# Optimization experiments

Measured on AMD Instinct MI355X. Metric: run time of the kernel, lower is better.

The kernel has to match this reference:

```python
import jax, jax.numpy as jnp
import numpy as np
from jax import lax

B, T, I, H = 256, 256, 512, 512


def setup_inputs() -> dict:
    key = jax.random.key(0)
    ks = jax.random.split(key, 7)
    s = 1.0 / np.sqrt(H)
    return {
        "x": jax.random.normal(ks[0], (B, T, I), dtype=jnp.float32),
        "W_ih": jax.random.normal(ks[1], (4 * H, I), dtype=jnp.float32) * s,
        "W_hh": jax.random.normal(ks[2], (4 * H, H), dtype=jnp.float32) * s,
        "b_ih": jax.random.normal(ks[3], (4 * H,), dtype=jnp.float32) * s,
        "b_hh": jax.random.normal(ks[4], (4 * H,), dtype=jnp.float32) * s,
        "fc_w": jax.random.normal(ks[5], (1, H), dtype=jnp.float32) * s,
        "fc_b": jax.random.normal(ks[6], (1,), dtype=jnp.float32) * s,
    }


def reference(x, W_ih, W_hh, b_ih, b_hh, fc_w, fc_b):
    # x: [B, T, I]. Single-layer LSTM (PyTorch gate order i,f,g,o), zero init state.
    Bh = x.shape[0]
    Hd = W_hh.shape[1]
    # Precompute input contribution for all timesteps: [B, T, 4H]
    xg = jnp.einsum('bti,gi->btg', x, W_ih) + b_ih + b_hh

    def step(carry, xt):
        h, c = carry
        g = xt + h @ W_hh.T  # [B, 4H]
        i = jax.nn.sigmoid(g[:, :Hd])
        f = jax.nn.sigmoid(g[:, Hd:2 * Hd])
        gg = jnp.tanh(g[:, 2 * Hd:3 * Hd])
        o = jax.nn.sigmoid(g[:, 3 * Hd:])
        c_new = f * c + i * gg
        h_new = o * jnp.tanh(c_new)
        return (h_new, c_new), None

    h0 = jnp.zeros((Bh, Hd), dtype=x.dtype)
    c0 = jnp.zeros((Bh, Hd), dtype=x.dtype)
    (h_last, _), _ = lax.scan(step, (h0, c0), jnp.swapaxes(xg, 0, 1))
    # Final linear head on last timestep: [B, 1]
    return h_last @ fc_w.T + fc_b
```

## Files before the change

### kernel.cpp

```cpp
#include <hip/hip_runtime.h>

#define BDIM 256
#define TDIM 256
#define IDIM 512
#define HDIM 512
#define G4   2048

#define HBW64 32768ull
#define SENT  0x7FC07FC07FC07FC0ull

typedef __attribute__((ext_vector_type(4))) float f32x4;
typedef __attribute__((ext_vector_type(8))) short short8;
typedef __attribute__((ext_vector_type(8))) unsigned short u16x8;
typedef __attribute__((ext_vector_type(4))) unsigned short u16x4;
typedef unsigned long long ull;

__device__ __forceinline__ unsigned short f2bf(float f) {
  union { float f; unsigned u; } v; v.f = f;
  unsigned r = v.u + 0x7FFFu + ((v.u >> 16) & 1u);
  return (unsigned short)(r >> 16);
}
__device__ __forceinline__ float bf2f(unsigned short h) {
  union { unsigned u; float f; } v; v.u = ((unsigned)h) << 16; return v.f;
}
__device__ __forceinline__ float sigmoidf_fast(float x) {
  return 1.0f / (1.0f + __expf(-x));
}
__device__ __forceinline__ float tanhf_fast(float x) {
  float e = __expf(2.0f * x);
  return 1.0f - 2.0f / (e + 1.0f);
}
__device__ __forceinline__ void gl_lds16(const unsigned short* g, unsigned short* l) {
  __builtin_amdgcn_global_load_lds(
      (const __attribute__((address_space(1))) unsigned int*)g,
      (__attribute__((address_space(3))) unsigned int*)l, 16, 0, 0);
}

__device__ __forceinline__ size_t xg_off(int m, int n) {
  int b = m >> 8, t = m & 255;
  int q = n >> 9, jcol = n & 511;
  return (((size_t)t * 8 + (b >> 5)) * 8 + (jcol >> 6)) * 8192
         + (size_t)q * 2048 + (b & 31) * 64 + (jcol & 63);
}

__global__ void __launch_bounds__(256) convert_bf16(
    const float* __restrict__ x, const float* __restrict__ w,
    unsigned short* __restrict__ xb, unsigned short* __restrict__ wb)
{
  const size_t NX8 = (size_t)BDIM * TDIM * IDIM / 8;
  const size_t NW8 = (size_t)G4 * IDIM / 8;
  size_t idx = (size_t)blockIdx.x * 256 + threadIdx.x;
  const float4* sp; u16x8* dp; size_t i;
  if (idx < NX8)      { sp = (const float4*)x; dp = (u16x8*)xb; i = idx; }
  else if (idx < NX8 + NW8) { sp = (const float4*)w; dp = (u16x8*)wb; i = idx - NX8; }
  else return;
  float4 a = sp[i * 2], b = sp[i * 2 + 1];
  u16x8 o = { f2bf(a.x), f2bf(a.y), f2bf(a.z), f2bf(a.w),
              f2bf(b.x), f2bf(b.y), f2bf(b.z), f2bf(b.w) };
  dp[i] = o;
}

__global__ void __launch_bounds__(256) init_bufs(unsigned short* __restrict__ hb)
{
  size_t i = (size_t)blockIdx.x * 256 + threadIdx.x;
  ull* b = (ull*)hb;
  if (i < HBW64)            b[i] = SENT;
  else if (i < 2 * HBW64)   b[3 * HBW64 + (i - HBW64)] = 0ull;
}

__global__ void __launch_bounds__(256, 2) xg_gemm_bf16(
    const unsigned short* __restrict__ Xb, const unsigned short* __restrict__ Wb,
    const float* __restrict__ b_ih, const float* __restrict__ b_hh,
    unsigned short* __restrict__ xg)
{
  __shared__ unsigned short sA[128 * 32];
  __shared__ unsigned short sB[128 * 32];

  const int tid  = threadIdx.x;
  const int lane = tid & 63;
  const int wave = tid >> 6;
  const int l15  = lane & 15;
  const int quad = lane >> 4;
  const int nt = blockIdx.x & 15;
  const int mt = blockIdx.x >> 4;
  const int wm = (wave >> 1) * 64;
  const int wn = (wave & 1) * 64;

  f32x4 acc[4][4];
  #pragma unroll
  for (int i = 0; i < 4; ++i)
    #pragma unroll
    for (int j = 0; j < 4; ++j)
      acc[i][j] = (f32x4){0.f, 0.f, 0.f, 0.f};

  for (int kt = 0; kt < 16; ++kt) {
    #pragma unroll
    for (int i = 0; i < 2; ++i) {
      int c   = wave * 128 + i * 64 + lane;
      int row = c >> 2, cg = c & 3;
      const unsigned short* ga = Xb + (size_t)(mt * 128 + row) * 512 + kt * 32 + cg * 8;
      gl_lds16(ga, sA + (size_t)(wave * 128 + i * 64) * 8);
      const unsigned short* gb = Wb + (size_t)(nt * 128 + row) * 512 + kt * 32 + cg * 8;
      gl_lds16(gb, sB + (size_t)(wave * 128 + i * 64) * 8);
    }
    __syncthreads();

    short8 af[4], bfr[4];
    #pragma unroll
    for (int i = 0; i < 4; ++i) {
      af[i]  = *(const short8*)&sA[(wm + i * 16 + l15) * 32 + quad * 8];
      bfr[i] = *(const short8*)&sB[(wn + i * 16 + l15) * 32 + quad * 8];
    }
    #pragma unroll
    for (int am = 0; am < 4; ++am)
      #pragma unroll
      for (int an = 0; an < 4; ++an)
        acc[am][an] = __builtin_amdgcn_mfma_f32_16x16x32_bf16(
            af[am], bfr[an], acc[am][an], 0, 0, 0);
    __syncthreads();
  }

  float biasv[4];
  #pragma unroll
  for (int an = 0; an < 4; ++an) {
    int n = nt * 128 + wn + an * 16 + l15;
    biasv[an] = b_ih[n] + b_hh[n];
  }
  #pragma unroll
  for (int am = 0; am < 4; ++am)
    #pragma unroll
    for (int reg = 0; reg < 4; ++reg) {
      int m = mt * 128 + wm + am * 16 + quad * 4 + reg;
      #pragma unroll
      for (int an = 0; an < 4; ++an) {
        int n = nt * 128 + wn + an * 16 + l15;
        __builtin_nontemporal_store(f2bf(acc[am][an][reg] + biasv[an]),
                                    &xg[xg_off(m, n)]);
      }
    }
}

__global__ void __launch_bounds__(256, 2) xg_gemm_f32(
    const float* __restrict__ X, const float* __restrict__ Wih,
    const float* __restrict__ b_ih, const float* __restrict__ b_hh,
    unsigned short* __restrict__ xg)
{
  __shared__ unsigned short sA[128][40];
  __shared__ unsigned short sB[128][40];

  const int tid  = threadIdx.x;
  const int lane = tid & 63;
  const int wave = tid >> 6;
  const int l15  = lane & 15;
  const int quad = lane >> 4;
  const int nt = blockIdx.x;
  const int mt = blockIdx.y;
  const int wm = (wave >> 1) * 64;
  const int wn = (wave & 1) * 64;
  const int r    = tid >> 1;
  const int half = (tid & 1) * 16;

  const float* arow = X   + (size_t)(mt * 128 + r) * 512 + half;
  const float* brow = Wih + (size_t)(nt * 128 + r) * 512 + half;

  f32x4 acc[4][4];
  #pragma unroll
  for (int i = 0; i < 4; ++i)
    #pragma unroll
    for (int j = 0; j < 4; ++j)
      acc[i][j] = (f32x4){0.f, 0.f, 0.f, 0.f};

  for (int kt = 0; kt < 16; ++kt) {
    const float* ap = arow + kt * 32;
    const float* bp = brow + kt * 32;
    #pragma unroll
    for (int i = 0; i < 4; ++i) {
      float4 a = ((const float4*)ap)[i];
      u16x4 av = { f2bf(a.x), f2bf(a.y), f2bf(a.z), f2bf(a.w) };
      *(u16x4*)&sA[r][half + i * 4] = av;
      float4 b = ((const float4*)bp)[i];
      u16x4 bv = { f2bf(b.x), f2bf(b.y), f2bf(b.z), f2bf(b.w) };
      *(u16x4*)&sB[r][half + i * 4] = bv;
    }
    __syncthreads();
    short8 af[4], bfr[4];
    #pragma unroll
    for (int i = 0; i < 4; ++i) {
      af[i]  = *(const short8*)&sA[wm + i * 16 + l15][quad * 8];
      bfr[i] = *(const short8*)&sB[wn + i * 16 + l15][quad * 8];
    }
    #pragma unroll
    for (int am = 0; am < 4; ++am)
      #pragma unroll
      for (int an = 0; an < 4; ++an)
        acc[am][an] = __builtin_amdgcn_mfma_f32_16x16x32_bf16(
            af[am], bfr[an], acc[am][an], 0, 0, 0);
    __syncthreads();
  }

  float biasv[4];
  #pragma unroll
  for (int an = 0; an < 4; ++an) {
    int n = nt * 128 + wn + an * 16 + l15;
    biasv[an] = b_ih[n] + b_hh[n];
  }
  #pragma unroll
  for (int am = 0; am < 4; ++am)
    #pragma unroll
    for (int reg = 0; reg < 4; ++reg) {
      int m = mt * 128 + wm + am * 16 + quad * 4 + reg;
      #pragma unroll
      for (int an = 0; an < 4; ++an) {
        int n = nt * 128 + wn + an * 16 + l15;
        __builtin_nontemporal_store(f2bf(acc[am][an][reg] + biasv[an]),
                                    &xg[xg_off(m, n)]);
      }
    }
}

__global__ void __launch_bounds__(512, 2) lstm_scan(
    const float* __restrict__ Whh, const unsigned short* __restrict__ xg,
    unsigned short* __restrict__ hb)
{
  __shared__ unsigned short sH[32][520];
  __shared__ float sG[32][260];

  const int tid  = threadIdx.x;
  const int lane = tid & 63;
  const int wave = tid >> 6;
  const int l15  = lane & 15;
  const int quad = lane >> 4;
  const int q    = wave >> 1;
  const int np   = (wave & 1) * 2;
  const int bb = blockIdx.x >> 3;
  const int jw = blockIdx.x & 7;
  const int bbase = bb * 32;
  const int jbase = jw * 64;

  short8 bfrag[2][16];
  #pragma unroll
  for (int n2 = 0; n2 < 2; ++n2) {
    const float* wrow = Whh + (size_t)(q * 512 + jbase + (np + n2) * 16 + l15) * 512;
    #pragma unroll
    for (int ks = 0; ks < 16; ++ks) {
      const float* p = wrow + ks * 32 + quad * 8;
      float4 f0 = ((const float4*)p)[0];
      float4 f1 = ((const float4*)p)[1];
      short8 v;
      v[0] = (short)f2bf(f0.x); v[1] = (short)f2bf(f0.y);
      v[2] = (short)f2bf(f0.z); v[3] = (short)f2bf(f0.w);
      v[4] = (short)f2bf(f1.x); v[5] = (short)f2bf(f1.y);
      v[6] = (short)f2bf(f1.z); v[7] = (short)f2bf(f1.w);
      bfrag[n2][ks] = v;
    }
  }

  const int r  = tid >> 4;
  const int j0 = (tid & 15) * 4;
  float c[4] = {0.f, 0.f, 0.f, 0.f};

  ull* hb64 = (ull*)hb;
  const size_t myw = (size_t)(bbase + r) * 128 + (size_t)((jbase + j0) >> 2);

  for (int t = 0; t < TDIM; ++t) {
    const ull* srcb = hb64 + (size_t)((t + 3) & 3) * HBW64;
    ull*       dstb = hb64 + (size_t)(t & 3) * HBW64;

    if (t < TDIM - 2) {
      ull* wipb = hb64 + (size_t)((t + 1) & 3) * HBW64;
      __hip_atomic_store(wipb + myw, SENT, __ATOMIC_RELAXED,
                         __HIP_MEMORY_SCOPE_AGENT);
    }

    const unsigned short* xgb = xg + (((size_t)t * 8 + bb) * 8 + jw) * 8192;
    ull xv64[4];
    #pragma unroll
    for (int qq = 0; qq < 4; ++qq)
      xv64[qq] = __builtin_nontemporal_load(
          (const ull*)(xgb + qq * 2048 + r * 64 + j0));

    const ull* src = srcb + (size_t)bbase * 128;
    ull hv[8];
    #pragma unroll
    for (int i = 0; i < 8; ++i)
      hv[i] = __hip_atomic_load(src + i * 512 + tid, __ATOMIC_RELAXED,
                                __HIP_MEMORY_SCOPE_AGENT);
    for (int guard = 0; guard < (1 << 18); ++guard) {
      int bad = 0;
      #pragma unroll
      for (int i = 0; i < 8; ++i) bad |= (int)(hv[i] == SENT) << i;
      if (!bad) break;
      __builtin_amdgcn_s_sleep(1);
      #pragma unroll
      for (int i = 0; i < 8; ++i)
        if (bad & (1 << i))
          hv[i] = __hip_atomic_load(src + i * 512 + tid, __ATOMIC_RELAXED,
                                    __HIP_MEMORY_SCOPE_AGENT);
    }
    #pragma unroll
    for (int i = 0; i < 8; ++i) {
      int idx = i * 512 + tid;
      *(ull*)&sH[idx >> 7][(idx & 127) * 4] = hv[i];
    }
    __syncthreads();

    f32x4 acc[2][2];
    acc[0][0] = acc[0][1] = acc[1][0] = acc[1][1] = (f32x4){0.f,0.f,0.f,0.f};
    #pragma unroll
    for (int ks = 0; ks < 16; ++ks) {
      int koff = ks * 32 + quad * 8;
      short8 a0 = *(const short8*)&sH[l15][koff];
      short8 a1 = *(const short8*)&sH[16 + l15][koff];
      acc[0][0] = __builtin_amdgcn_mfma_f32_16x16x32_bf16(a0, bfrag[0][ks], acc[0][0], 0, 0, 0);
      acc[1][0] = __builtin_amdgcn_mfma_f32_16x16x32_bf16(a1, bfrag[0][ks], acc[1][0], 0, 0, 0);
      acc[0][1] = __builtin_amdgcn_mfma_f32_16x16x32_bf16(a0, bfrag[1][ks], acc[0][1], 0, 0, 0);
      acc[1][1] = __builtin_amdgcn_mfma_f32_16x16x32_bf16(a1, bfrag[1][ks], acc[1][1], 0, 0, 0);
    }
    #pragma unroll
    for (int m = 0; m < 2; ++m)
      #pragma unroll
      for (int n2 = 0; n2 < 2; ++n2) {
        int col = q * 64 + (np + n2) * 16 + l15;
        #pragma unroll
        for (int rr = 0; rr < 4; ++rr)
          sG[m * 16 + quad * 4 + rr][col] = acc[m][n2][rr];
      }
    __syncthreads();

    {
      float4 GI = *(const float4*)&sG[r][j0];
      float4 GF = *(const float4*)&sG[r][64 + j0];
      float4 GG = *(const float4*)&sG[r][128 + j0];
      float4 GO = *(const float4*)&sG[r][192 + j0];
      u16x4 xi  = __builtin_bit_cast(u16x4, xv64[0]);
      u16x4 xf  = __builtin_bit_cast(u16x4, xv64[1]);
      u16x4 xgv = __builtin_bit_cast(u16x4, xv64[2]);
      u16x4 xo  = __builtin_bit_cast(u16x4, xv64[3]);
      float gi[4] = {GI.x, GI.y, GI.z, GI.w};
      float gf[4] = {GF.x, GF.y, GF.z, GF.w};
      float gg[4] = {GG.x, GG.y, GG.z, GG.w};
      float go[4] = {GO.x, GO.y, GO.z, GO.w};
      float h4[4];
      #pragma unroll
      for (int k = 0; k < 4; ++k) {
        float vi = sigmoidf_fast(gi[k] + bf2f(xi[k]));
        float vf = sigmoidf_fast(gf[k] + bf2f(xf[k]));
        float vg = tanhf_fast   (gg[k] + bf2f(xgv[k]));
        float vo = sigmoidf_fast(go[k] + bf2f(xo[k]));
        c[k] = vf * c[k] + vi * vg;
        h4[k] = vo * tanhf_fast(c[k]);
      }
      ull hvout = (ull)f2bf(h4[0])
                | ((ull)f2bf(h4[1]) << 16)
                | ((ull)f2bf(h4[2]) << 32)
                | ((ull)f2bf(h4[3]) << 48);
      asm volatile("s_waitcnt vmcnt(0)" ::: "memory");
      __hip_atomic_store(dstb + myw, hvout, __ATOMIC_RELAXED,
                         __HIP_MEMORY_SCOPE_AGENT);
    }
  }
}

__global__ void head_kernel(const unsigned short* __restrict__ h,
                            const float* __restrict__ fc_w,
                            const float* __restrict__ fc_b,
                            float* __restrict__ out)
{
  const int b = blockIdx.x;
  const int lane = threadIdx.x;
  const unsigned short* hr = h + (size_t)b * 512;
  float s = 0.f;
  #pragma unroll
  for (int i = 0; i < 8; ++i) {
    int idx = lane + i * 64;
    s += bf2f(hr[idx]) * fc_w[idx];
  }
  #pragma unroll
  for (int off = 32; off > 0; off >>= 1) s += __shfl_down(s, off);
  if (lane == 0) out[b] = s + fc_b[0];
}

extern "C" void kernel_launch(void* const* d_in, const int* in_sizes, int n_in,
                              void* d_out, int out_size, void* d_ws, size_t ws_size,
                              hipStream_t stream) {
  const float* x    = (const float*)d_in[0];
  const float* W_ih = (const float*)d_in[1];
  const float* W_hh = (const float*)d_in[2];
  const float* b_ih = (const float*)d_in[3];
  const float* b_hh = (const float*)d_in[4];
  const float* fc_w = (const float*)d_in[5];
  const float* fc_b = (const float*)d_in[6];
  float* out = (float*)d_out;

  const size_t XG  = (size_t)BDIM * TDIM * G4 * 2;
  char* ws = (char*)d_ws;
  unsigned short* xg = (unsigned short*)ws;
  unsigned short* hb = (unsigned short*)(ws + XG);
  const size_t XB_OFF = XG;
  const size_t WB_OFF = XG + (size_t)BDIM * TDIM * IDIM * 2;
  const size_t NEED   = WB_OFF + (size_t)G4 * IDIM * 2;

  if (ws_size >= NEED) {
    unsigned short* xb = (unsigned short*)(ws + XB_OFF);
    unsigned short* wb = (unsigned short*)(ws + WB_OFF);
    convert_bf16<<<16896, 256, 0, stream>>>(x, W_ih, xb, wb);
    xg_gemm_bf16<<<8192, 256, 0, stream>>>(xb, wb, b_ih, b_hh, xg);
  } else {
    xg_gemm_f32<<<dim3(16, 512), 256, 0, stream>>>(x, W_ih, b_ih, b_hh, xg);
  }
  init_bufs<<<256, 256, 0, stream>>>(hb);
  lstm_scan<<<64, 512, 0, stream>>>(W_hh, xg, hb);
  head_kernel<<<BDIM, 64, 0, stream>>>(hb + 3 * (size_t)HBW64 * 4, fc_w, fc_b, out);
}
```

Measured before the change: 1.486 ms.

## Use L2-coherent plain stores and atomic-add reads for inter-block h exchange

Adds a startup handshake that checks whether blocks sharing a batch slice can see each other's plain global stores through L2. When they can, it switches the per-step hidden-state exchange to plain dwordx2 stores and returns-value atomic_add(0) reads, which bypass the non-coherent cache path and should lower per-step communication latency. Otherwise it falls back to the old agent-scope atomics on a second buffer set. The block-to-tile mapping is also swapped so the 8 blocks of one batch slice are strided across the grid. This adds a probe phase at startup and depends on hardware cache behaviour, with a possible hang or mismatch if the probe gives a wrong answer.

```diff
diff --git a/kernel.cpp b/kernel.cpp
--- a/kernel.cpp
+++ b/kernel.cpp
@@ -8,6 +8,8 @@
 
 #define HBW64 32768ull
 #define SENT  0x7FC07FC07FC07FC0ull
+#define TOK1  0xA5A5A5A5A5A5A5A5ull
+#define TOK2  0x5A5A5A5A5A5A5A5Aull
 
 typedef __attribute__((ext_vector_type(4))) float f32x4;
 typedef __attribute__((ext_vector_type(8))) short short8;
@@ -34,6 +36,20 @@
   __builtin_amdgcn_global_load_lds(
       (const __attribute__((address_space(1))) unsigned int*)g,
       (__attribute__((address_space(3))) unsigned int*)l, 16, 0, 0);
+}
+__device__ __forceinline__ void store64_l2(ull* p, ull v) {
+  asm volatile("global_store_dwordx2 %0, %1, off" :: "v"(p), "v"(v) : "memory");
+}
+__device__ __forceinline__ void read64_l2_issue(ull* p, ull* dst) {
+  asm volatile("global_atomic_add_x2 %0, %1, %2, off sc0"
+               : "=&v"(*dst) : "v"(p), "v"(0ull) : "memory");
+}
+__device__ __forceinline__ void vm_drain() {
+  asm volatile("s_waitcnt vmcnt(0)" ::: "memory");
+  __builtin_amdgcn_sched_barrier(0);
+}
+__device__ __forceinline__ ull read64_l2(ull* p) {
+  ull v; read64_l2_issue(p, &v); vm_drain(); return v;
 }
 
 __device__ __forceinline__ size_t xg_off(int m, int n) {
@@ -60,12 +76,14 @@
   dp[i] = o;
 }
 
-__global__ void __launch_bounds__(256) init_bufs(unsigned short* __restrict__ hb)
+__global__ void __launch_bounds__(256) init_bufs(ull* __restrict__ hb,
+    ull* __restrict__ ftest, unsigned* __restrict__ fres)
 {
   size_t i = (size_t)blockIdx.x * 256 + threadIdx.x;
-  ull* b = (ull*)hb;
-  if (i < HBW64)            b[i] = SENT;
-  else if (i < 2 * HBW64)   b[3 * HBW64 + (i - HBW64)] = 0ull;
+  if (i < HBW64)          { hb[i] = SENT; hb[4 * HBW64 + i] = SENT; }
+  else if (i < 2 * HBW64) { size_t j = i - HBW64;
+                            hb[3 * HBW64 + j] = 0ull; hb[7 * HBW64 + j] = 0ull; }
+  if (i < 64) { ftest[i] = 0ull; fres[i] = 0xFFFFFFFFu; }
 }
 
 __global__ void __launch_bounds__(256, 2) xg_gemm_bf16(
@@ -220,10 +238,12 @@
 
 __global__ void __launch_bounds__(512, 2) lstm_scan(
     const float* __restrict__ Whh, const unsigned short* __restrict__ xg,
-    unsigned short* __restrict__ hb)
+    ull* __restrict__ hbF, ull* __restrict__ hbS,
+    ull* __restrict__ ftest, unsigned* __restrict__ fres)
 {
   __shared__ unsigned short sH[32][520];
   __shared__ float sG[32][260];
+  __shared__ int sT, sF;
 
   const int tid  = threadIdx.x;
   const int lane = tid & 63;
@@ -232,10 +252,15 @@
   const int quad = lane >> 4;
   const int q    = wave >> 1;
   const int np   = (wave & 1) * 2;
-  const int bb = blockIdx.x >> 3;
-  const int jw = blockIdx.x & 7;
+  const int bb = blockIdx.x & 7;
+  const int jw = blockIdx.x >> 3;
   const int bbase = bb * 32;
   const int jbase = jw * 64;
+
+  if (tid == 0) {
+    store64_l2(ftest + blockIdx.x, TOK1);
+    asm volatile("s_waitcnt vmcnt(0)" ::: "memory");
+  }
 
   short8 bfrag[2][16];
   #pragma unroll
@@ -255,21 +280,83 @@
     }
   }
 
+  {
+    int r1 = 0, r2 = 0;
+    if (wave == 0) {
+      ull v = 0;
+      if (lane < 8) {
+        ull* p = ftest + (lane * 8 + bb);
+        for (int g = 0; g < (1 << 13); ++g) {
+          v = read64_l2(p);
+          if (v == TOK1 || v == TOK2) break;
+          __builtin_amdgcn_s_sleep(2);
+        }
+      }
+      int ok = (lane >= 8) || (((v == TOK1) | (v == TOK2)) != 0);
+      ull m = __ballot(ok);
+      if (lane == 0) sT = ((m & 0xFFull) == 0xFFull) ? 1 : 0;
+    }
+    __syncthreads();
+    r1 = sT;
+    if (r1 && tid == 0) {
+      store64_l2(ftest + blockIdx.x, TOK2);
+      asm volatile("s_waitcnt vmcnt(0)" ::: "memory");
+    }
+    __syncthreads();
+    if (r1) {
+      if (wave == 0) {
+        ull v = 0;
+        if (lane < 8) {
+          ull* p = ftest + (lane * 8 + bb);
+          for (int g = 0; g < (1 << 13); ++g) {
+            v = read64_l2(p);
+            if (v == TOK2) break;
+            __builtin_amdgcn_s_sleep(2);
+          }
+        }
+        int ok = (lane >= 8) || (v == TOK2);
+        ull m = __ballot(ok);
+        if (lane == 0) sT = ((m & 0xFFull) == 0xFFull) ? 1 : 0;
+      }
+      __syncthreads();
+      r2 = sT;
+    }
+    if (tid == 0)
+      __hip_atomic_store(fres + blockIdx.x, (unsigned)(r1 && r2),
+                         __ATOMIC_RELAXED, __HIP_MEMORY_SCOPE_AGENT);
+    if (wave == 0) {
+      unsigned v = 0xFFFFFFFFu;
+      if (lane < 8) {
+        const unsigned* p = fres + (lane * 8 + bb);
+        for (int g = 0; g < (1 << 18); ++g) {
+          v = __hip_atomic_load(p, __ATOMIC_RELAXED, __HIP_MEMORY_SCOPE_AGENT);
+          if (v != 0xFFFFFFFFu) break;
+          __builtin_amdgcn_s_sleep(2);
+        }
+      }
+      int ok = (lane >= 8) || (v == 1u);
+      ull m = __ballot(ok);
+      if (lane == 0) sF = ((m & 0xFFull) == 0xFFull) ? 1 : 0;
+    }
+    __syncthreads();
+  }
+  const int fastok = sF;
+
   const int r  = tid >> 4;
   const int j0 = (tid & 15) * 4;
   float c[4] = {0.f, 0.f, 0.f, 0.f};
 
-  ull* hb64 = (ull*)hb;
   const size_t myw = (size_t)(bbase + r) * 128 + (size_t)((jbase + j0) >> 2);
 
   for (int t = 0; t < TDIM; ++t) {
-    const ull* srcb = hb64 + (size_t)((t + 3) & 3) * HBW64;
-    ull*       dstb = hb64 + (size_t)(t & 3) * HBW64;
+    const size_t sb = (size_t)((t + 3) & 3) * HBW64;
+    const size_t db = (size_t)(t & 3) * HBW64;
 
     if (t < TDIM - 2) {
-      ull* wipb = hb64 + (size_t)((t + 1) & 3) * HBW64;
-      __hip_atomic_store(wipb + myw, SENT, __ATOMIC_RELAXED,
-                         __HIP_MEMORY_SCOPE_AGENT);
+      const size_t wb = (size_t)((t + 1) & 3) * HBW64;
+      if (fastok) store64_l2(hbF + wb + myw, SENT);
+      else        __hip_atomic_store(hbS + wb + myw, SENT, __ATOMIC_RELAXED,
+                                     __HIP_MEMORY_SCOPE_AGENT);
     }
 
     const unsigned short* xgb = xg + (((size_t)t * 8 + bb) * 8 + jw) * 8192;
@@ -279,23 +366,44 @@
       xv64[qq] = __builtin_nontemporal_load(
           (const ull*)(xgb + qq * 2048 + r * 64 + j0));
 
-    const ull* src = srcb + (size_t)bbase * 128;
     ull hv[8];
-    #pragma unroll
-    for (int i = 0; i < 8; ++i)
-      hv[i] = __hip_atomic_load(src + i * 512 + tid, __ATOMIC_RELAXED,
-                                __HIP_MEMORY_SCOPE_AGENT);
-    for (int guard = 0; guard < (1 << 18); ++guard) {
-      int bad = 0;
-      #pragma unroll
-      for (int i = 0; i < 8; ++i) bad |= (int)(hv[i] == SENT) << i;
-      if (!bad) break;
-      __builtin_amdgcn_s_sleep(1);
+    if (fastok) {
+      ull* sp = hbF + sb + (size_t)bbase * 128 + tid;
+      #pragma unroll
+      for (int i = 0; i < 4; ++i) read64_l2_issue(sp + (size_t)i * 512, &hv[i]);
+      vm_drain();
+      #pragma unroll
+      for (int i = 4; i < 8; ++i) read64_l2_issue(sp + (size_t)i * 512, &hv[i]);
+      vm_drain();
+      for (int guard = 0; guard < (1 << 18); ++guard) {
+        int bad = 0;
+        #pragma unroll
+        for (int i = 0; i < 8; ++i) bad |= (int)(hv[i] == SENT) << i;
+        if (!bad) break;
+        __builtin_amdgcn_s_sleep(1);
+        #pragma unroll
+        for (int i = 0; i < 8; ++i)
+          if (bad & (1 << i)) read64_l2_issue(sp + (size_t)i * 512, &hv[i]);
+        vm_drain();
+      }
+    } else {
+      const ull* sp = hbS + sb + (size_t)bbase * 128 + tid;
       #pragma unroll
       for (int i = 0; i < 8; ++i)
-        if (bad & (1 << i))
-          hv[i] = __hip_atomic_load(src + i * 512 + tid, __ATOMIC_RELAXED,
-                                    __HIP_MEMORY_SCOPE_AGENT);
+        hv[i] = __hip_atomic_load(sp + (size_t)i * 512, __ATOMIC_RELAXED,
+                                  __HIP_MEMORY_SCOPE_AGENT);
+      for (int guard = 0; guard < (1 << 18); ++guard) {
+        int bad = 0;
+        #pragma unroll
+        for (int i = 0; i < 8; ++i) bad |= (int)(hv[i] == SENT) << i;
+        if (!bad) break;
+        __builtin_amdgcn_s_sleep(1);
+        #pragma unroll
+        for (int i = 0; i < 8; ++i)
+          if (bad & (1 << i))
+            hv[i] = __hip_atomic_load(sp + (size_t)i * 512, __ATOMIC_RELAXED,
+                                      __HIP_MEMORY_SCOPE_AGENT);
+      }
     }
     #pragma unroll
     for (int i = 0; i < 8; ++i) {
@@ -354,9 +462,11 @@
                 | ((ull)f2bf(h4[1]) << 16)
                 | ((ull)f2bf(h4[2]) << 32)
                 | ((ull)f2bf(h4[3]) << 48);
-      asm volatile("s_waitcnt vmcnt(0)" ::: "memory");
-      __hip_atomic_store(dstb + myw, hvout, __ATOMIC_RELAXED,
-                         __HIP_MEMORY_SCOPE_AGENT);
+      vm_drain();
+      store64_l2(hbF + db + myw, hvout);
+      if (!fastok)
+        __hip_atomic_store(hbS + db + myw, hvout, __ATOMIC_RELAXED,
+                           __HIP_MEMORY_SCOPE_AGENT);
     }
   }
 }
@@ -395,7 +505,11 @@
   const size_t XG  = (size_t)BDIM * TDIM * G4 * 2;
   char* ws = (char*)d_ws;
   unsigned short* xg = (unsigned short*)ws;
-  unsigned short* hb = (unsigned short*)(ws + XG);
+  ull* hbF = (ull*)(ws + XG);
+  ull* hbS = hbF + 4 * HBW64;
+  char* aux = ws + XG + 8 * HBW64 * 8;
+  ull*      ftest = (ull*)aux;
+  unsigned* fres  = (unsigned*)(aux + 512);
   const size_t XB_OFF = XG;
   const size_t WB_OFF = XG + (size_t)BDIM * TDIM * IDIM * 2;
   const size_t NEED   = WB_OFF + (size_t)G4 * IDIM * 2;
@@ -408,7 +522,8 @@
   } else {
     xg_gemm_f32<<<dim3(16, 512), 256, 0, stream>>>(x, W_ih, b_ih, b_hh, xg);
   }
-  init_bufs<<<256, 256, 0, stream>>>(hb);
-  lstm_scan<<<64, 512, 0, stream>>>(W_hh, xg, hb);
-  head_kernel<<<BDIM, 64, 0, stream>>>(hb + 3 * (size_t)HBW64 * 4, fc_w, fc_b, out);
-}
+  init_bufs<<<256, 256, 0, stream>>>(hbF, ftest, fres);
+  lstm_scan<<<64, 512, 0, stream>>>(W_hh, xg, hbF, hbS, ftest, fres);
+  head_kernel<<<BDIM, 64, 0, stream>>>((const unsigned short*)(hbF + 3 * HBW64),
+                                       fc_w, fc_b, out);
+}
```

New measurement: 1.560 ms. 5.0% more time.
